# Optimization experiments

Hardware: AMD Instinct MI355X
Metric: run time of the kernel (lower is better)

## Reference

```python
import jax, jax.numpy as jnp
import numpy as np

N_BASIS = 16
CUTOFF = 5.0
S3 = 3.0 ** 0.5


def _cg_121():
    # Real Clebsch-Gordan for 1o x 2e -> 1o built from the equivariant map
    # (v, T) -> T @ v where T is the traceless symmetric matrix encoded by the
    # 5 real l=2 components (e3nn y-principal convention). Normalized to unit
    # Frobenius norm (wigner-3j-like normalization).
    s15 = np.sqrt(15.0); s5 = np.sqrt(5.0)
    C = np.zeros((3, 3, 5))
    for j in range(5):
        c = np.zeros(5); c[j] = 1.0
        T = np.zeros((3, 3))
        T[0, 2] = T[2, 0] = c[0] / s15
        T[0, 1] = T[1, 0] = c[1] / s15
        T[1, 2] = T[2, 1] = c[3] / s15
        Tyy = 2.0 * c[2] / (3.0 * s5)
        T[1, 1] = Tyy
        T[2, 2] = -Tyy / 2.0 + c[4] / s15
        T[0, 0] = -Tyy / 2.0 - c[4] / s15
        C[:, :, j] = T
    C /= np.linalg.norm(C)
    return jnp.asarray(C, dtype=jnp.float32)


def _sph(n):
    # component-normalized real spherical harmonics l=0,1,2 of unit vectors n [E,3]
    x, y, z = n[:, 0], n[:, 1], n[:, 2]
    Y0 = jnp.ones_like(x)
    Y1 = S3 * n  # [E,3]
    s15 = 15.0 ** 0.5; s5 = 5.0 ** 0.5
    Y2 = jnp.stack([s15 * x * z, s15 * x * y, 0.5 * s5 * (3 * y * y - 1.0),
                    s15 * y * z, 0.5 * s15 * (z * z - x * x)], axis=-1)  # [E,5]
    return Y0, Y1, Y2


def _tfn_forward(x, pos, W1, W2, edge_index, cg121):
    row, col = edge_index[0], edge_index[1]
    E = row.shape[0]
    N = pos.shape[0]
    ev = pos[row] - pos[col]                         # [E,3]
    d = jnp.sqrt(jnp.sum(ev * ev, axis=-1) + 1e-12)  # [E]
    n = ev / d[:, None]
    # Gaussian radial basis, 16 centers on [0, cutoff]
    mu = jnp.linspace(0.0, CUTOFF, N_BASIS)
    delta = CUTOFF / (N_BASIS - 1)
    rbf = jnp.exp(-((d[:, None] - mu) ** 2) / (2.0 * delta * delta))  # [E,16]
    # normalized 2-layer MLP -> per-edge TP weights [E, 576]
    h = jax.nn.relu((rbf @ W1) / jnp.sqrt(16.0))
    w = (h @ W2) / jnp.sqrt(64.0)
    Y0, Y1, Y2 = _sph(n)
    ss = jnp.stack([Y0, Y0], axis=-1)   # [E,2]  2x0e
    sv = jnp.stack([Y1, Y1], axis=1)    # [E,2,3] 2x1o
    st = Y2                              # [E,5]  1x2e
    xs = x[row, :8]                      # [E,8]  8x0e
    xv = x[row, 8:].reshape(E, 8, 3)     # [E,8,3] 8x1o
    wA = w[:, 0:128].reshape(E, 8, 2, 8)
    wB = w[:, 128:256].reshape(E, 8, 2, 8)
    wC = w[:, 256:384].reshape(E, 8, 2, 8)
    wD = w[:, 384:512].reshape(E, 8, 2, 8)
    wE = w[:, 512:576].reshape(E, 8, 8)
    a0 = 1.0 / jnp.sqrt(32.0)            # sqrt(2*0+1)/sqrt(fan_in=32)
    a1 = jnp.sqrt(3.0) / jnp.sqrt(40.0)  # sqrt(2*1+1)/sqrt(fan_in=40)
    out_s = a0 * (jnp.einsum('euvw,eu,ev->ew', wA, xs, ss)
                  + jnp.einsum('euvw,eui,evi->ew', wB, xv, sv) / S3)
    out_v = a1 * (jnp.einsum('euvw,eu,evk->ewk', wC, xs, sv) / S3
                  + jnp.einsum('euvw,euk,ev->ewk', wD, xv, ss) / S3
                  + jnp.einsum('euw,eui,ej,kij->ewk', wE, xv, st, cg121))
    out = jnp.concatenate([out_s, out_v.reshape(E, 24)], axis=-1)  # [E,32]
    y = jax.ops.segment_sum(out, row, num_segments=N)              # [N,32]
    # gate: silu on scalar (l=0) channels only
    return jnp.concatenate([jax.nn.silu(y[:, :8]), y[:, 8:]], axis=-1)


def setup_inputs() -> dict:
    key = jax.random.key(0)
    k1, k2, k3, k4, k5 = jax.random.split(key, 5)
    N, E = 25000, 400000
    x = jax.random.normal(k1, (N, 32), dtype=jnp.float32)
    pos = jax.random.normal(k2, (N, 3), dtype=jnp.float32)
    edge_index = jax.random.randint(k3, (2, E), 0, N, dtype=jnp.int64 if jax.config.read('jax_enable_x64') else jnp.int32)
    W1 = jax.random.normal(k4, (16, 64), dtype=jnp.float32)
    W2 = jax.random.normal(k5, (64, 576), dtype=jnp.float32)
    return {"x": x, "pos": pos, "edge_index": edge_index, "W1": W1, "W2": W2}


def reference(x, pos, edge_index, W1, W2):
    cg121 = _cg_121()
    return _tfn_forward(x, pos, W1, W2, edge_index, cg121)
```

## Files before the change

kernel.cpp:

```cpp
#include <hip/hip_runtime.h>
#include <hip/hip_fp16.h>


#define INV_S3  0.5773502691896258f
#define A0S     0.1767766952966369f
#define A1S     0.27386127875258306f
#define S15     3.872983346207417f
#define S5      2.23606797749979f
#define INV_S10 0.31622776601683794f
#define INV_S30 0.18257418583505536f

#define TBL   4096
#define RPB   16
#define BBLK  (TBL / RPB)
#define GRID  2048
#define DMAX  8.0f
#define CAP   64
#define CSTR  16

typedef _Float16 half8 __attribute__((ext_vector_type(8)));
typedef _Float16 half2v __attribute__((ext_vector_type(2)));

__global__ __launch_bounds__(256) void prep_all(
    const float* __restrict__ W1, const float* __restrict__ W2,
    const int* __restrict__ ei, const float* __restrict__ pos,
    _Float16* __restrict__ T, int* __restrict__ cnt,
    uint2* __restrict__ srec, int E) {

    __shared__ float hs[RPB][64];
    int tid = threadIdx.x;
    int wv = tid >> 6, lane = tid & 63;

    if (blockIdx.x < BBLK) {
        int jb = blockIdx.x * RPB;
#pragma unroll
        for (int s = 0; s < 4; ++s) {
            int j = jb + wv * 4 + s;
            float d = (float)j * (DMAX / (float)(TBL - 1));
            float acc = 0.f;
#pragma unroll
            for (int i = 0; i < 16; ++i) {
                float t = d - (float)i * (1.0f / 3.0f);
                float r = __expf(-4.5f * t * t);
                acc = fmaf(r, W1[i * 64 + lane], acc);
            }
            hs[wv * 4 + s][lane] = fmaxf(acc, 0.f) * 0.25f;
        }
        __syncthreads();

        int u = lane >> 3, wo = lane & 7;
        int b0 = u * 16 + wo;
        int b4 = 512 + u * 8 + wo;
        float a0[4] = {0.f, 0.f, 0.f, 0.f};
        float a1[4] = {0.f, 0.f, 0.f, 0.f};
        float a2[4] = {0.f, 0.f, 0.f, 0.f};
        float a3[4] = {0.f, 0.f, 0.f, 0.f};
        float a4[4] = {0.f, 0.f, 0.f, 0.f};
#pragma unroll 2
        for (int k = 0; k < 64; ++k) {
            const float* Wk = W2 + k * 576;
            float w0 = Wk[b0]       + Wk[b0 + 8];
            float w1 = Wk[128 + b0] + Wk[128 + b0 + 8];
            float w2 = Wk[256 + b0] + Wk[256 + b0 + 8];
            float w3 = Wk[384 + b0] + Wk[384 + b0 + 8];
            float w4 = Wk[b4];
#pragma unroll
            for (int s = 0; s < 4; ++s) {
                float hk = hs[wv * 4 + s][k];
                a0[s] = fmaf(hk, w0, a0[s]);
                a1[s] = fmaf(hk, w1, a1[s]);
                a2[s] = fmaf(hk, w2, a2[s]);
                a3[s] = fmaf(hk, w3, a3[s]);
                a4[s] = fmaf(hk, w4, a4[s]);
            }
        }
#pragma unroll
        for (int s = 0; s < 4; ++s) {
            int j = jb + wv * 4 + s;
            _Float16* Tr = T + (size_t)j * 320;
            int base = u * 16 + wo * 2;
            Tr[base]             = (_Float16)a0[s];
            Tr[base + 1]         = (_Float16)a1[s];
            Tr[128 + base]       = (_Float16)a2[s];
            Tr[128 + base + 1]   = (_Float16)a3[s];
            Tr[256 + u * 8 + wo] = (_Float16)a4[s];
        }
    } else {
        int gtid = (blockIdx.x - BBLK) * 256 + tid;
        int gsz = (GRID - BBLK) * 256;
        for (int e = gtid; e < E; e += gsz) {
            int row = ei[e];
            int col = ei[E + e];
            float ax = pos[3 * row + 0] - pos[3 * col + 0];
            float ay = pos[3 * row + 1] - pos[3 * col + 1];
            float az = pos[3 * row + 2] - pos[3 * col + 2];
            float d2 = ax * ax + ay * ay + az * az + 1e-12f;
            float invd = rsqrtf(d2);
            float dd = d2 * invd;
            int p = atomicAdd(&cnt[(size_t)row * CSTR], 1);
            if (p < CAP) {
                __half2 h0 = __floats2half2_rn(ax * invd, ay * invd);
                __half2 h1 = __floats2half2_rn(az * invd, dd);
                uint2 r;
                r.x = *(const unsigned*)&h0;
                r.y = *(const unsigned*)&h1;
                srec[(size_t)row * CAP + p] = r;
            }
        }
    }
}

__global__ __launch_bounds__(64) void tfn_node(
    const float* __restrict__ x, const uint2* __restrict__ srec,
    const int* __restrict__ cnt, const _Float16* __restrict__ T,
    float* __restrict__ y, int N) {

    int lane = threadIdx.x & 63;
    int n = blockIdx.x;
    if (n >= N) return;

    int g = lane >> 3;
    int u = lane & 7;
    int kc = cnt[(size_t)n * CSTR];
    if (kc > CAP) kc = CAP;
    const uint2* recs = srec + (size_t)n * CAP;

    const float* xr = x + (size_t)n * 32;
    float xu  = xr[u];
    float xv0 = xr[8 + 3 * u + 0];
    float xv1 = xr[8 + 3 * u + 1];
    float xv2 = xr[8 + 3 * u + 2];
    _Float16 xuh = (_Float16)xu;
    _Float16 p30 = (_Float16)(xv0 * INV_S3);
    _Float16 p31 = (_Float16)(xv1 * INV_S3);
    _Float16 p32 = (_Float16)(xv2 * INV_S3);

    float V[32];
#pragma unroll
    for (int z = 0; z < 32; ++z) V[z] = 0.f;

    int rounds = (kc + 7) >> 3;
    uint2 rec = make_uint2(0u, 0u);
    if (rounds > 0) rec = recs[g];
    for (int rd = 0; rd < rounds; ++rd) {
        uint2 cur = rec;
        int slot = rd * 8 + g;
        if (rd + 1 < rounds) rec = recs[slot + 8];
        if (slot < kc) {
            __half2 h0 = *(const __half2*)&cur.x;
            __half2 h1 = *(const __half2*)&cur.y;
            float2 f0 = __half22float2(h0);
            float2 f1 = __half22float2(h1);
            float nx = f0.x, ny = f0.y, nz = f1.x;
            float dd = f1.y;

            float fj = dd * ((float)(TBL - 1) / DMAX);
            int j0 = (int)(fj + 0.5f);
            j0 = min(j0, TBL - 1);

            const _Float16* Ar = T + (size_t)j0 * 320;
            const _Float16* Au = Ar + u * 16;
            half8 w01a = *(const half8*)(Au);
            half8 w01b = *(const half8*)(Au + 8);
            half8 w23a = *(const half8*)(Au + 128);
            half8 w23b = *(const half8*)(Au + 136);
            half8 w4l  = *(const half8*)(Ar + 256 + u * 8);

            float qu = xv0 * nx + xv1 * ny + xv2 * nz;
            float Y22 = 0.5f * S5 * (3.f * ny * ny - 1.f);
            float Y24 = 0.5f * S15 * (nz * nz - nx * nx);
            float M00 = -Y22 * INV_S30 - Y24 * INV_S10;
            float M11 = 2.f * Y22 * INV_S30;
            float M22 = -Y22 * INV_S30 + Y24 * INV_S10;
            float M01 = (S15 * nx * ny) * INV_S10;
            float M02 = (S15 * nx * nz) * INV_S10;
            float M12 = (S15 * ny * nz) * INV_S10;
            float m0 = M00 * xv0 + M01 * xv1 + M02 * xv2;
            float m1 = M01 * xv0 + M11 * xv1 + M12 * xv2;
            float m2 = M02 * xv0 + M12 * xv1 + M22 * xv2;

            half2v xq;  xq.x = xuh;  xq.y = (_Float16)qu;
            half2v c0;  c0.x = (_Float16)(xu * nx);  c0.y = p30;
            half2v c1;  c1.x = (_Float16)(xu * ny);  c1.y = p31;
            half2v c2;  c2.x = (_Float16)(xu * nz);  c2.y = p32;

#pragma unroll
            for (int z = 0; z < 4; ++z) {
                half2v pa; pa.x = w01a[2 * z]; pa.y = w01a[2 * z + 1];
                V[z] = __builtin_amdgcn_fdot2(pa, xq, V[z], false);
                half2v pb; pb.x = w01b[2 * z]; pb.y = w01b[2 * z + 1];
                V[4 + z] = __builtin_amdgcn_fdot2(pb, xq, V[4 + z], false);
            }

#pragma unroll
            for (int z = 0; z < 4; ++z) {
                half2v pa; pa.x = w23a[2 * z]; pa.y = w23a[2 * z + 1];
                int b = 8 + 3 * z;
                V[b]     = __builtin_amdgcn_fdot2(pa, c0, V[b],     false);
                V[b + 1] = __builtin_amdgcn_fdot2(pa, c1, V[b + 1], false);
                V[b + 2] = __builtin_amdgcn_fdot2(pa, c2, V[b + 2], false);
                half2v pb; pb.x = w23b[2 * z]; pb.y = w23b[2 * z + 1];
                int b2 = 8 + 3 * (z + 4);
                V[b2]     = __builtin_amdgcn_fdot2(pb, c0, V[b2],     false);
                V[b2 + 1] = __builtin_amdgcn_fdot2(pb, c1, V[b2 + 1], false);
                V[b2 + 2] = __builtin_amdgcn_fdot2(pb, c2, V[b2 + 2], false);
            }

#pragma unroll
            for (int z = 0; z < 8; ++z) {
                float we = (float)w4l[z];
                V[8 + 3 * z]  = fmaf(m0, we, V[8 + 3 * z]);
                V[9 + 3 * z]  = fmaf(m1, we, V[9 + 3 * z]);
                V[10 + 3 * z] = fmaf(m2, we, V[10 + 3 * z]);
            }
        }
    }

#pragma unroll
    for (int h = 16; h >= 1; h >>= 1) {
        bool hi = (lane & h) != 0;
#pragma unroll
        for (int k = 0; k < h; ++k) {
            float lo = V[k], up = V[k + h];
            float keep = hi ? up : lo;
            float send = hi ? lo : up;
            V[k] = keep + __shfl_xor(send, h, 64);
        }
    }
    V[0] += __shfl_xor(V[0], 32, 64);

    if (lane < 32) {
        float v = V[0] * 0.125f * (lane < 8 ? A0S : A1S);
        if (lane < 8) v = v / (1.0f + __expf(-v));
        y[(size_t)n * 32 + lane] = v;
    }
}

extern "C" void kernel_launch(void* const* d_in, const int* in_sizes, int n_in,
                              void* d_out, int out_size, void* d_ws, size_t ws_size,
                              hipStream_t stream) {
    const float* x   = (const float*)d_in[0];
    const float* pos = (const float*)d_in[1];
    const int*   ei  = (const int*)d_in[2];
    const float* W1  = (const float*)d_in[3];
    const float* W2  = (const float*)d_in[4];
    int N = in_sizes[1] / 3;
    int E = in_sizes[2] / 2;

    char* ws = (char*)d_ws;
    size_t off = 0;
    _Float16* T    = (_Float16*)(ws + off); off += (size_t)TBL * 320 * 2;
    int*      cnt  = (int*)(ws + off);      off += (size_t)N * CSTR * 4;
    uint2*    srec = (uint2*)(ws + off);    off += (size_t)N * CAP * 8;

    float* y = (float*)d_out;

    hipMemsetAsync(cnt, 0, (size_t)N * CSTR * 4, stream);
    hipLaunchKernelGGL(prep_all, dim3(GRID), dim3(256), 0, stream,
                       W1, W2, ei, pos, T, cnt, srec, E);
    hipLaunchKernelGGL(tfn_node, dim3(N), dim3(64), 0, stream,
                       x, srec, cnt, T, y, N);
}
```

Baseline: 121.6 us.

## Split node range in halves to overlap edge scatter with node compute

The edge scatter is split by destination row into two halves. The first kernel builds the table and scatters first-half edges. A second kernel scatters second-half edges while its other blocks compute first-half nodes, and a third kernel computes the second-half nodes. The goal is to overlap scatter work with node compute across kernel boundaries. The cost is that each scatter pass must read the full edge list twice, and there is an extra kernel launch.

```diff
diff --git a/kernel.cpp b/kernel.cpp
--- a/kernel.cpp
+++ b/kernel.cpp
@@ -13,7 +13,8 @@
 #define TBL   4096
 #define RPB   16
 #define BBLK  (TBL / RPB)
-#define GRID  2048
+#define SBLK1 1024
+#define SBLK2 2048
 #define DMAX  8.0f
 #define CAP   64
 #define CSTR  16
@@ -21,11 +22,158 @@
 typedef _Float16 half8 __attribute__((ext_vector_type(8)));
 typedef _Float16 half2v __attribute__((ext_vector_type(2)));
 
-__global__ __launch_bounds__(256) void prep_all(
+__device__ __forceinline__ void scatter_edge(
+    int e, int lo, int hi, const int* __restrict__ ei,
+    const float* __restrict__ pos, int* __restrict__ cnt,
+    uint2* __restrict__ srec, int E) {
+    int row = ei[e];
+    if (row >= lo && row < hi) {
+        int col = ei[E + e];
+        float ax = pos[3 * row + 0] - pos[3 * col + 0];
+        float ay = pos[3 * row + 1] - pos[3 * col + 1];
+        float az = pos[3 * row + 2] - pos[3 * col + 2];
+        float d2 = ax * ax + ay * ay + az * az + 1e-12f;
+        float invd = rsqrtf(d2);
+        float dd = d2 * invd;
+        int p = atomicAdd(&cnt[(size_t)row * CSTR], 1);
+        if (p < CAP) {
+            __half2 h0 = __floats2half2_rn(ax * invd, ay * invd);
+            __half2 h1 = __floats2half2_rn(az * invd, dd);
+            uint2 r;
+            r.x = *(const unsigned*)&h0;
+            r.y = *(const unsigned*)&h1;
+            srec[(size_t)row * CAP + p] = r;
+        }
+    }
+}
+
+__device__ __forceinline__ void node_body(
+    int n, int lane, const float* __restrict__ x,
+    const uint2* __restrict__ srec, const int* __restrict__ cnt,
+    const _Float16* __restrict__ T, float* __restrict__ y) {
+
+    int g = lane >> 3;
+    int u = lane & 7;
+    int kc = cnt[(size_t)n * CSTR];
+    if (kc > CAP) kc = CAP;
+    const uint2* recs = srec + (size_t)n * CAP;
+
+    const float* xr = x + (size_t)n * 32;
+    float xu  = xr[u];
+    float xv0 = xr[8 + 3 * u + 0];
+    float xv1 = xr[8 + 3 * u + 1];
+    float xv2 = xr[8 + 3 * u + 2];
+    _Float16 xuh = (_Float16)xu;
+    _Float16 p30 = (_Float16)(xv0 * INV_S3);
+    _Float16 p31 = (_Float16)(xv1 * INV_S3);
+    _Float16 p32 = (_Float16)(xv2 * INV_S3);
+
+    float V[32];
+#pragma unroll
+    for (int z = 0; z < 32; ++z) V[z] = 0.f;
+
+    int rounds = (kc + 7) >> 3;
+    uint2 rec = make_uint2(0u, 0u);
+    if (rounds > 0) rec = recs[g];
+    for (int rd = 0; rd < rounds; ++rd) {
+        uint2 cur = rec;
+        int slot = rd * 8 + g;
+        if (rd + 1 < rounds) rec = recs[slot + 8];
+        if (slot < kc) {
+            __half2 h0 = *(const __half2*)&cur.x;
+            __half2 h1 = *(const __half2*)&cur.y;
+            float2 f0 = __half22float2(h0);
+            float2 f1 = __half22float2(h1);
+            float nx = f0.x, ny = f0.y, nz = f1.x;
+            float dd = f1.y;
+
+            float fj = dd * ((float)(TBL - 1) / DMAX);
+            int j0 = (int)(fj + 0.5f);
+            j0 = min(j0, TBL - 1);
+
+            const _Float16* Ar = T + (size_t)j0 * 320;
+            const _Float16* Au = Ar + u * 16;
+            half8 w01a = *(const half8*)(Au);
+            half8 w01b = *(const half8*)(Au + 8);
+            half8 w23a = *(const half8*)(Au + 128);
+            half8 w23b = *(const half8*)(Au + 136);
+            half8 w4l  = *(const half8*)(Ar + 256 + u * 8);
+
+            float qu = xv0 * nx + xv1 * ny + xv2 * nz;
+            float Y22 = 0.5f * S5 * (3.f * ny * ny - 1.f);
+            float Y24 = 0.5f * S15 * (nz * nz - nx * nx);
+            float M00 = -Y22 * INV_S30 - Y24 * INV_S10;
+            float M11 = 2.f * Y22 * INV_S30;
+            float M22 = -Y22 * INV_S30 + Y24 * INV_S10;
+            float M01 = (S15 * nx * ny) * INV_S10;
+            float M02 = (S15 * nx * nz) * INV_S10;
+            float M12 = (S15 * ny * nz) * INV_S10;
+            float m0 = M00 * xv0 + M01 * xv1 + M02 * xv2;
+            float m1 = M01 * xv0 + M11 * xv1 + M12 * xv2;
+            float m2 = M02 * xv0 + M12 * xv1 + M22 * xv2;
+
+            half2v xq;  xq.x = xuh;  xq.y = (_Float16)qu;
+            half2v c0;  c0.x = (_Float16)(xu * nx);  c0.y = p30;
+            half2v c1;  c1.x = (_Float16)(xu * ny);  c1.y = p31;
+            half2v c2;  c2.x = (_Float16)(xu * nz);  c2.y = p32;
+
+#pragma unroll
+            for (int z = 0; z < 4; ++z) {
+                half2v pa; pa.x = w01a[2 * z]; pa.y = w01a[2 * z + 1];
+                V[z] = __builtin_amdgcn_fdot2(pa, xq, V[z], false);
+                half2v pb; pb.x = w01b[2 * z]; pb.y = w01b[2 * z + 1];
+                V[4 + z] = __builtin_amdgcn_fdot2(pb, xq, V[4 + z], false);
+            }
+
+#pragma unroll
+            for (int z = 0; z < 4; ++z) {
+                half2v pa; pa.x = w23a[2 * z]; pa.y = w23a[2 * z + 1];
+                int b = 8 + 3 * z;
+                V[b]     = __builtin_amdgcn_fdot2(pa, c0, V[b],     false);
+                V[b + 1] = __builtin_amdgcn_fdot2(pa, c1, V[b + 1], false);
+                V[b + 2] = __builtin_amdgcn_fdot2(pa, c2, V[b + 2], false);
+                half2v pb; pb.x = w23b[2 * z]; pb.y = w23b[2 * z + 1];
+                int b2 = 8 + 3 * (z + 4);
+                V[b2]     = __builtin_amdgcn_fdot2(pb, c0, V[b2],     false);
+                V[b2 + 1] = __builtin_amdgcn_fdot2(pb, c1, V[b2 + 1], false);
+                V[b2 + 2] = __builtin_amdgcn_fdot2(pb, c2, V[b2 + 2], false);
+            }
+
+#pragma unroll
+            for (int z = 0; z < 8; ++z) {
+                float we = (float)w4l[z];
+                V[8 + 3 * z]  = fmaf(m0, we, V[8 + 3 * z]);
+                V[9 + 3 * z]  = fmaf(m1, we, V[9 + 3 * z]);
+                V[10 + 3 * z] = fmaf(m2, we, V[10 + 3 * z]);
+            }
+        }
+    }
+
+#pragma unroll
+    for (int h = 16; h >= 1; h >>= 1) {
+        bool hi = (lane & h) != 0;
+#pragma unroll
+        for (int k = 0; k < h; ++k) {
+            float lo = V[k], up = V[k + h];
+            float keep = hi ? up : lo;
+            float send = hi ? lo : up;
+            V[k] = keep + __shfl_xor(send, h, 64);
+        }
+    }
+    V[0] += __shfl_xor(V[0], 32, 64);
+
+    if (lane < 32) {
+        float v = V[0] * 0.125f * (lane < 8 ? A0S : A1S);
+        if (lane < 8) v = v / (1.0f + __expf(-v));
+        y[(size_t)n * 32 + lane] = v;
+    }
+}
+
+__global__ __launch_bounds__(256) void prep_A(
     const float* __restrict__ W1, const float* __restrict__ W2,
     const int* __restrict__ ei, const float* __restrict__ pos,
     _Float16* __restrict__ T, int* __restrict__ cnt,
-    uint2* __restrict__ srec, int E) {
+    uint2* __restrict__ srec, int E, int NH) {
 
     __shared__ float hs[RPB][64];
     int tid = threadIdx.x;
@@ -87,153 +235,39 @@
         }
     } else {
         int gtid = (blockIdx.x - BBLK) * 256 + tid;
-        int gsz = (GRID - BBLK) * 256;
-        for (int e = gtid; e < E; e += gsz) {
-            int row = ei[e];
-            int col = ei[E + e];
-            float ax = pos[3 * row + 0] - pos[3 * col + 0];
-            float ay = pos[3 * row + 1] - pos[3 * col + 1];
-            float az = pos[3 * row + 2] - pos[3 * col + 2];
-            float d2 = ax * ax + ay * ay + az * az + 1e-12f;
-            float invd = rsqrtf(d2);
-            float dd = d2 * invd;
-            int p = atomicAdd(&cnt[(size_t)row * CSTR], 1);
-            if (p < CAP) {
-                __half2 h0 = __floats2half2_rn(ax * invd, ay * invd);
-                __half2 h1 = __floats2half2_rn(az * invd, dd);
-                uint2 r;
-                r.x = *(const unsigned*)&h0;
-                r.y = *(const unsigned*)&h1;
-                srec[(size_t)row * CAP + p] = r;
-            }
-        }
-    }
-}
-
-__global__ __launch_bounds__(64) void tfn_node(
+        int gsz = SBLK1 * 256;
+        for (int e = gtid; e < E; e += gsz)
+            scatter_edge(e, 0, NH, ei, pos, cnt, srec, E);
+    }
+}
+
+__global__ __launch_bounds__(64) void scat_node(
+    const float* __restrict__ x, const float* __restrict__ pos,
+    const int* __restrict__ ei, _Float16* __restrict__ T,
+    int* __restrict__ cnt, uint2* __restrict__ srec,
+    float* __restrict__ y, int E, int N, int NH) {
+
+    int lane = threadIdx.x & 63;
+    if (blockIdx.x < SBLK2) {
+        int gtid = blockIdx.x * 64 + lane;
+        const int gsz = SBLK2 * 64;
+        for (int e = gtid; e < E; e += gsz)
+            scatter_edge(e, NH, N, ei, pos, cnt, srec, E);
+    } else {
+        int n = blockIdx.x - SBLK2;
+        node_body(n, lane, x, srec, cnt, T, y);
+    }
+}
+
+__global__ __launch_bounds__(64) void node_B(
     const float* __restrict__ x, const uint2* __restrict__ srec,
     const int* __restrict__ cnt, const _Float16* __restrict__ T,
-    float* __restrict__ y, int N) {
+    float* __restrict__ y, int N, int NH) {
 
     int lane = threadIdx.x & 63;
-    int n = blockIdx.x;
+    int n = NH + blockIdx.x;
     if (n >= N) return;
-
-    int g = lane >> 3;
-    int u = lane & 7;
-    int kc = cnt[(size_t)n * CSTR];
-    if (kc > CAP) kc = CAP;
-    const uint2* recs = srec + (size_t)n * CAP;
-
-    const float* xr = x + (size_t)n * 32;
-    float xu  = xr[u];
-    float xv0 = xr[8 + 3 * u + 0];
-    float xv1 = xr[8 + 3 * u + 1];
-    float xv2 = xr[8 + 3 * u + 2];
-    _Float16 xuh = (_Float16)xu;
-    _Float16 p30 = (_Float16)(xv0 * INV_S3);
-    _Float16 p31 = (_Float16)(xv1 * INV_S3);
-    _Float16 p32 = (_Float16)(xv2 * INV_S3);
-
-    float V[32];
-#pragma unroll
-    for (int z = 0; z < 32; ++z) V[z] = 0.f;
-
-    int rounds = (kc + 7) >> 3;
-    uint2 rec = make_uint2(0u, 0u);
-    if (rounds > 0) rec = recs[g];
-    for (int rd = 0; rd < rounds; ++rd) {
-        uint2 cur = rec;
-        int slot = rd * 8 + g;
-        if (rd + 1 < rounds) rec = recs[slot + 8];
-        if (slot < kc) {
-            __half2 h0 = *(const __half2*)&cur.x;
-            __half2 h1 = *(const __half2*)&cur.y;
-            float2 f0 = __half22float2(h0);
-            float2 f1 = __half22float2(h1);
-            float nx = f0.x, ny = f0.y, nz = f1.x;
-            float dd = f1.y;
-
-            float fj = dd * ((float)(TBL - 1) / DMAX);
-            int j0 = (int)(fj + 0.5f);
-            j0 = min(j0, TBL - 1);
-
-            const _Float16* Ar = T + (size_t)j0 * 320;
-            const _Float16* Au = Ar + u * 16;
-            half8 w01a = *(const half8*)(Au);
-            half8 w01b = *(const half8*)(Au + 8);
-            half8 w23a = *(const half8*)(Au + 128);
-            half8 w23b = *(const half8*)(Au + 136);
-            half8 w4l  = *(const half8*)(Ar + 256 + u * 8);
-
-            float qu = xv0 * nx + xv1 * ny + xv2 * nz;
-            float Y22 = 0.5f * S5 * (3.f * ny * ny - 1.f);
-            float Y24 = 0.5f * S15 * (nz * nz - nx * nx);
-            float M00 = -Y22 * INV_S30 - Y24 * INV_S10;
-            float M11 = 2.f * Y22 * INV_S30;
-            float M22 = -Y22 * INV_S30 + Y24 * INV_S10;
-            float M01 = (S15 * nx * ny) * INV_S10;
-            float M02 = (S15 * nx * nz) * INV_S10;
-            float M12 = (S15 * ny * nz) * INV_S10;
-            float m0 = M00 * xv0 + M01 * xv1 + M02 * xv2;
-            float m1 = M01 * xv0 + M11 * xv1 + M12 * xv2;
-            float m2 = M02 * xv0 + M12 * xv1 + M22 * xv2;
-
-            half2v xq;  xq.x = xuh;  xq.y = (_Float16)qu;
-            half2v c0;  c0.x = (_Float16)(xu * nx);  c0.y = p30;
-            half2v c1;  c1.x = (_Float16)(xu * ny);  c1.y = p31;
-            half2v c2;  c2.x = (_Float16)(xu * nz);  c2.y = p32;
-
-#pragma unroll
-            for (int z = 0; z < 4; ++z) {
-                half2v pa; pa.x = w01a[2 * z]; pa.y = w01a[2 * z + 1];
-                V[z] = __builtin_amdgcn_fdot2(pa, xq, V[z], false);
-                half2v pb; pb.x = w01b[2 * z]; pb.y = w01b[2 * z + 1];
-                V[4 + z] = __builtin_amdgcn_fdot2(pb, xq, V[4 + z], false);
-            }
-
-#pragma unroll
-            for (int z = 0; z < 4; ++z) {
-                half2v pa; pa.x = w23a[2 * z]; pa.y = w23a[2 * z + 1];
-                int b = 8 + 3 * z;
-                V[b]     = __builtin_amdgcn_fdot2(pa, c0, V[b],     false);
-                V[b + 1] = __builtin_amdgcn_fdot2(pa, c1, V[b + 1], false);
-                V[b + 2] = __builtin_amdgcn_fdot2(pa, c2, V[b + 2], false);
-                half2v pb; pb.x = w23b[2 * z]; pb.y = w23b[2 * z + 1];
-                int b2 = 8 + 3 * (z + 4);
-                V[b2]     = __builtin_amdgcn_fdot2(pb, c0, V[b2],     false);
-                V[b2 + 1] = __builtin_amdgcn_fdot2(pb, c1, V[b2 + 1], false);
-                V[b2 + 2] = __builtin_amdgcn_fdot2(pb, c2, V[b2 + 2], false);
-            }
-
-#pragma unroll
-            for (int z = 0; z < 8; ++z) {
-                float we = (float)w4l[z];
-                V[8 + 3 * z]  = fmaf(m0, we, V[8 + 3 * z]);
-                V[9 + 3 * z]  = fmaf(m1, we, V[9 + 3 * z]);
-                V[10 + 3 * z] = fmaf(m2, we, V[10 + 3 * z]);
-            }
-        }
-    }
-
-#pragma unroll
-    for (int h = 16; h >= 1; h >>= 1) {
-        bool hi = (lane & h) != 0;
-#pragma unroll
-        for (int k = 0; k < h; ++k) {
-            float lo = V[k], up = V[k + h];
-            float keep = hi ? up : lo;
-            float send = hi ? lo : up;
-            V[k] = keep + __shfl_xor(send, h, 64);
-        }
-    }
-    V[0] += __shfl_xor(V[0], 32, 64);
-
-    if (lane < 32) {
-        float v = V[0] * 0.125f * (lane < 8 ? A0S : A1S);
-        if (lane < 8) v = v / (1.0f + __expf(-v));
-        y[(size_t)n * 32 + lane] = v;
-    }
+    node_body(n, lane, x, srec, cnt, T, y);
 }
 
 extern "C" void kernel_launch(void* const* d_in, const int* in_sizes, int n_in,
@@ -246,6 +280,7 @@
     const float* W2  = (const float*)d_in[4];
     int N = in_sizes[1] / 3;
     int E = in_sizes[2] / 2;
+    int NH = (N + 1) / 2;
 
     char* ws = (char*)d_ws;
     size_t off = 0;
@@ -256,8 +291,10 @@
     float* y = (float*)d_out;
 
     hipMemsetAsync(cnt, 0, (size_t)N * CSTR * 4, stream);
-    hipLaunchKernelGGL(prep_all, dim3(GRID), dim3(256), 0, stream,
-                       W1, W2, ei, pos, T, cnt, srec, E);
-    hipLaunchKernelGGL(tfn_node, dim3(N), dim3(64), 0, stream,
-                       x, srec, cnt, T, y, N);
-}
+    hipLaunchKernelGGL(prep_A, dim3(BBLK + SBLK1), dim3(256), 0, stream,
+                       W1, W2, ei, pos, T, cnt, srec, E, NH);
+    hipLaunchKernelGGL(scat_node, dim3(SBLK2 + NH), dim3(64), 0, stream,
+                       x, pos, ei, T, cnt, srec, y, E, N, NH);
+    hipLaunchKernelGGL(node_B, dim3(N - NH), dim3(64), 0, stream,
+                       x, srec, cnt, T, y, N, NH);
+}
```

Result: no change. 121.7 us (+0.1%).
